# Optimization experiments

Measured on AMD Instinct MI355X. Metric: run time of the kernel, lower is better.

The kernel has to match this reference:

```python
import jax, jax.numpy as jnp
import numpy as np


def setup_inputs() -> dict:
    key = jax.random.key(0)
    k1, k2 = jax.random.split(key, 2)
    N, HrWr, HW = 16, 4096, 1024
    num_levels, max_k = 3, 5
    return {
        "R_combined": jax.random.normal(k1, (N, HrWr, HW), dtype=jnp.float32),
        "k_logits": jax.random.normal(k2, (num_levels, max_k), dtype=jnp.float32),
        "temperature": jnp.array(1.0, dtype=jnp.float32),
        "max_k": 5,
        "num_levels": 3,
    }


def reference(R_combined, k_logits, temperature, max_k, num_levels):
    # --- gumbel-softmax over k choices (soft samples, as in F.gumbel_softmax) ---
    gkey = jax.random.key(42)
    u = jax.random.uniform(gkey, k_logits.shape, k_logits.dtype,
                           minval=1e-6, maxval=1.0 - 1e-6)
    gumbels = -jnp.log(-jnp.log(u))
    k_probs = jax.nn.softmax((k_logits + gumbels) / temperature, axis=-1)  # [L, max_k]
    k_hard = jnp.argmax(k_probs, axis=-1) + 1                              # [L] ints in [1, max_k]
    k_soft = jnp.sum(k_probs * jnp.arange(1, max_k + 1, dtype=k_probs.dtype), axis=-1)
    # straight-through estimator
    k_selected = (jax.lax.stop_gradient(k_hard.astype(k_soft.dtype))
                  + k_soft - jax.lax.stop_gradient(k_soft))

    # --- top-k over HrWr axis (dim=1); take max_k once, then per-level mask.
    # topk(k) + pad to max_k with (-inf, 0)  ==  topk(max_k) masked at rank >= k,
    # since top_k returns sorted-descending values (matches torch.topk sorted=True).
    x = jnp.swapaxes(R_combined, 1, 2)           # [N, HW, HrWr]
    vals, idx = jax.lax.top_k(x, max_k)          # [N, HW, max_k]
    vals = jnp.swapaxes(vals, 1, 2)              # [N, max_k, HW]
    idx = jnp.swapaxes(idx, 1, 2)                # [N, max_k, HW]

    rank = jnp.arange(max_k)                     # [max_k]
    mask = (rank[None, :] < k_hard[:, None])[:, None, :, None]  # [L, 1, max_k, 1]
    R_star_levels = jnp.where(mask, vals[None], -jnp.inf)       # [L, N, max_k, HW]
    R_idx_levels = jnp.where(mask, idx[None], 0)                # [L, N, max_k, HW]

    return (k_selected, R_star_levels, R_idx_levels)
```

## Files before the change

kernel.cpp:

```cpp
#include <hip/hip_runtime.h>
#include <math.h>
#include <float.h>
#include <stdint.h>

#define N_N   16
#define HRWR  4096
#define HW_   1024
#define LVLS  3
#define MAXK  5
#define SEGS  8
#define SEGLEN (HRWR / SEGS)
#define COLS  32

#define NEG_SENTINEL (-1.0e30f)

__device__ __forceinline__ unsigned rotl32(unsigned x, unsigned r) {
  return (x << r) | (x >> (32u - r));
}

__device__ __forceinline__ bool beats(float v, int i, float V, int I) {
  return (v > V) || (v == V && i < I);
}

__global__ __launch_bounds__(256)
void dynk_kernel(const float* __restrict__ R,
                 const float* __restrict__ k_logits,
                 const float* __restrict__ temperature,
                 float* __restrict__ out)
{
  __shared__ float    s_vals[SEGS][COLS][MAXK];
  __shared__ int      s_idx [SEGS][COLS][MAXK];
  __shared__ unsigned s_bits[LVLS * MAXK];
  __shared__ int      s_khard[LVLS];

  const int tid = threadIdx.x;
  const int c   = tid & (COLS - 1);
  const int s   = tid >> 5;
  const int b   = blockIdx.x;
  const int n   = b >> 5;
  const int hw  = ((b & 31) << 5) | c;

  if (tid < LVLS * MAXK) {
    unsigned x0 = 0u, x1 = (unsigned)tid;
    const unsigned k0 = 0u, k1 = 42u;
    const unsigned k2 = k0 ^ k1 ^ 0x1BD11BDAu;
    x0 += k0; x1 += k1;
#define TF_RND(rot) { x0 += x1; x1 = rotl32(x1, rot); x1 ^= x0; }
    TF_RND(13) TF_RND(15) TF_RND(26) TF_RND(6)  x0 += k1; x1 += k2 + 1u;
    TF_RND(17) TF_RND(29) TF_RND(16) TF_RND(24) x0 += k2; x1 += k0 + 2u;
    TF_RND(13) TF_RND(15) TF_RND(26) TF_RND(6)  x0 += k0; x1 += k1 + 3u;
    TF_RND(17) TF_RND(29) TF_RND(16) TF_RND(24) x0 += k1; x1 += k2 + 4u;
    TF_RND(13) TF_RND(15) TF_RND(26) TF_RND(6)  x0 += k2; x1 += k0 + 5u;
#undef TF_RND
    s_bits[tid] = x0 ^ x1;
  }
  __syncthreads();

  if (tid == 0) {
    const float T = temperature[0];
    for (int l = 0; l < LVLS; ++l) {
      float z[MAXK], p[MAXK];
      float zmax = -INFINITY;
      for (int k = 0; k < MAXK; ++k) {
        unsigned bits = s_bits[l * MAXK + k];
        float f = __uint_as_float((bits >> 9) | 0x3f800000u) - 1.0f;
        const float mn = 1e-6f;
        const float mx = 1.0f - 1e-6f;
        float u = fmaxf(mn, f * (mx - mn) + mn);
        float g = -logf(-logf(u));
        z[k] = (k_logits[l * MAXK + k] + g) / T;
        zmax = fmaxf(zmax, z[k]);
      }
      float sum = 0.0f;
      for (int k = 0; k < MAXK; ++k) { p[k] = expf(z[k] - zmax); sum += p[k]; }
      float pmax = -INFINITY; int arg = 0; float ksoft = 0.0f;
      for (int k = 0; k < MAXK; ++k) {
        p[k] = p[k] / sum;
        if (p[k] > pmax) { pmax = p[k]; arg = k; }
        ksoft += p[k] * (float)(k + 1);
      }
      const int khard = arg + 1;
      s_khard[l] = khard;
      if (b == 0) out[l] = ((float)khard + ksoft) - ksoft;
    }
  }

  float tv[MAXK];
  int   ti[MAXK];
#pragma unroll
  for (int k = 0; k < MAXK; ++k) { tv[k] = -INFINITY; ti[k] = 0x7fffffff; }

  const float* __restrict__ base =
      R + ((size_t)n * HRWR + (size_t)s * SEGLEN) * HW_ + hw;
  const int r0 = s * SEGLEN;

  for (int r = 0; r < SEGLEN; r += 8) {
    float v[8];
#pragma unroll
    for (int j = 0; j < 8; ++j) v[j] = base[(size_t)(r + j) * HW_];
#pragma unroll
    for (int j = 0; j < 8; ++j) {
      const float val = v[j];
      if (val > tv[MAXK - 1]) {
        tv[MAXK - 1] = val;
        ti[MAXK - 1] = r0 + r + j;
#pragma unroll
        for (int k = MAXK - 1; k > 0; --k) {
          if (tv[k] > tv[k - 1]) {
            float tf = tv[k]; tv[k] = tv[k - 1]; tv[k - 1] = tf;
            int   tt = ti[k]; ti[k] = ti[k - 1]; ti[k - 1] = tt;
          }
        }
      }
    }
  }

#pragma unroll
  for (int k = 0; k < MAXK; ++k) { s_vals[s][c][k] = tv[k]; s_idx[s][c][k] = ti[k]; }
  __syncthreads();

  if (tid < COLS) {
    const int cc = tid;
    float fv[MAXK]; int fi[MAXK];
#pragma unroll
    for (int k = 0; k < MAXK; ++k) { fv[k] = s_vals[0][cc][k]; fi[k] = s_idx[0][cc][k]; }
    for (int ss = 1; ss < SEGS; ++ss) {
#pragma unroll
      for (int k = 0; k < MAXK; ++k) {
        const float v = s_vals[ss][cc][k];
        const int   i = s_idx [ss][cc][k];
        if (beats(v, i, fv[MAXK - 1], fi[MAXK - 1])) {
          fv[MAXK - 1] = v; fi[MAXK - 1] = i;
#pragma unroll
          for (int k2 = MAXK - 1; k2 > 0; --k2) {
            if (beats(fv[k2], fi[k2], fv[k2 - 1], fi[k2 - 1])) {
              float tf = fv[k2]; fv[k2] = fv[k2 - 1]; fv[k2 - 1] = tf;
              int   tt = fi[k2]; fi[k2] = fi[k2 - 1]; fi[k2 - 1] = tt;
            }
          }
        }
      }
    }

    const int hww = ((b & 31) << 5) | cc;
    float* __restrict__ star = out + LVLS;
    float* __restrict__ idxo = out + LVLS + (size_t)LVLS * N_N * MAXK * HW_;
#pragma unroll
    for (int l = 0; l < LVLS; ++l) {
      const int kh = s_khard[l];
#pragma unroll
      for (int k = 0; k < MAXK; ++k) {
        const bool on = (k < kh);
        const size_t off = (((size_t)l * N_N + n) * MAXK + k) * HW_ + hww;
        star[off] = on ? fv[k] : NEG_SENTINEL;
        idxo[off] = on ? (float)fi[k] : 0.0f;
      }
    }
  }
}

extern "C" void kernel_launch(void* const* d_in, const int* in_sizes, int n_in,
                              void* d_out, int out_size, void* d_ws, size_t ws_size,
                              hipStream_t stream) {
  const float* R    = (const float*)d_in[0];
  const float* kl   = (const float*)d_in[1];
  const float* temp = (const float*)d_in[2];
  float* out = (float*)d_out;

  dynk_kernel<<<dim3(512), dim3(256), 0, stream>>>(R, kl, temp, out);
}
```

Measured before the change: 410.3 us.

## Split top-k into partial and final kernels for more parallelism

The single 512-block kernel becomes a two-stage split-K reduction. The first kernel launches 2048 blocks, each scanning 512 rows for 64 columns, and writes per-split top-5 candidates to workspace. A second kernel merges the 8 splits per column, computes the gumbel k_hard values and writes the masked outputs. This fills the GPU far better for a memory-bound 256MB read, at the cost of an extra launch and some workspace traffic. Each wavefront now reads 64 contiguous floats (256B) per row.

After: 410.6 us. About the same (+0.1%).

```diff
diff --git a/kernel.cpp b/kernel.cpp
--- a/kernel.cpp
+++ b/kernel.cpp
@@ -8,9 +8,11 @@
 #define HW_   1024
 #define LVLS  3
 #define MAXK  5
-#define SEGS  8
-#define SEGLEN (HRWR / SEGS)
-#define COLS  32
+
+#define SLICES   16
+#define RSPLIT   8
+#define K1_SEGS  4
+#define K1_SEGLEN 128
 
 #define NEG_SENTINEL (-1.0e30f)
 
@@ -22,23 +24,92 @@
   return (v > V) || (v == V && i < I);
 }
 
+__global__ __launch_bounds__(256, 6)
+void dynk_partial(const float* __restrict__ R, float2* __restrict__ ws)
+{
+  __shared__ float s_vals[K1_SEGS][64][MAXK];
+  __shared__ int   s_idx [K1_SEGS][64][MAXK];
+
+  const int tid   = threadIdx.x;
+  const int c     = tid & 63;
+  const int s     = tid >> 6;
+  const int b     = blockIdx.x;
+  const int rs    = b & (RSPLIT - 1);
+  const int slice = (b >> 3) & (SLICES - 1);
+  const int n     = b >> 7;
+
+  const int r0 = rs * 512 + s * K1_SEGLEN;
+  const float* __restrict__ base =
+      R + ((size_t)n * HRWR + r0) * HW_ + slice * 64 + c;
+
+  float tv[MAXK]; int ti[MAXK];
+#pragma unroll
+  for (int k = 0; k < MAXK; ++k) { tv[k] = -INFINITY; ti[k] = 0x7fffffff; }
+
+  for (int r = 0; r < K1_SEGLEN; r += 8) {
+    float v[8];
+#pragma unroll
+    for (int j = 0; j < 8; ++j) v[j] = base[(size_t)(r + j) * HW_];
+#pragma unroll
+    for (int j = 0; j < 8; ++j) {
+      const float val = v[j];
+      if (val > tv[MAXK - 1]) {
+        tv[MAXK - 1] = val;
+        ti[MAXK - 1] = r0 + r + j;
+#pragma unroll
+        for (int k = MAXK - 1; k > 0; --k) {
+          if (tv[k] > tv[k - 1]) {
+            float tf = tv[k]; tv[k] = tv[k - 1]; tv[k - 1] = tf;
+            int   tt = ti[k]; ti[k] = ti[k - 1]; ti[k - 1] = tt;
+          }
+        }
+      }
+    }
+  }
+
+#pragma unroll
+  for (int k = 0; k < MAXK; ++k) { s_vals[s][c][k] = tv[k]; s_idx[s][c][k] = ti[k]; }
+  __syncthreads();
+
+  if (tid < 64) {
+    const int cc = tid;
+    float fv[MAXK]; int fi[MAXK];
+#pragma unroll
+    for (int k = 0; k < MAXK; ++k) { fv[k] = s_vals[0][cc][k]; fi[k] = s_idx[0][cc][k]; }
+    for (int ss = 1; ss < K1_SEGS; ++ss) {
+#pragma unroll
+      for (int k = 0; k < MAXK; ++k) {
+        const float v = s_vals[ss][cc][k];
+        const int   i = s_idx [ss][cc][k];
+        if (beats(v, i, fv[MAXK - 1], fi[MAXK - 1])) {
+          fv[MAXK - 1] = v; fi[MAXK - 1] = i;
+#pragma unroll
+          for (int k2 = MAXK - 1; k2 > 0; --k2) {
+            if (beats(fv[k2], fi[k2], fv[k2 - 1], fi[k2 - 1])) {
+              float tf = fv[k2]; fv[k2] = fv[k2 - 1]; fv[k2 - 1] = tf;
+              int   tt = fi[k2]; fi[k2] = fi[k2 - 1]; fi[k2 - 1] = tt;
+            }
+          }
+        }
+      }
+    }
+    float2* __restrict__ dst = ws + ((size_t)b * 64 + cc) * MAXK;
+#pragma unroll
+    for (int k = 0; k < MAXK; ++k)
+      dst[k] = make_float2(fv[k], __int_as_float(fi[k]));
+  }
+}
+
 __global__ __launch_bounds__(256)
-void dynk_kernel(const float* __restrict__ R,
-                 const float* __restrict__ k_logits,
-                 const float* __restrict__ temperature,
-                 float* __restrict__ out)
+void dynk_final(const float2* __restrict__ ws,
+                const float* __restrict__ k_logits,
+                const float* __restrict__ temperature,
+                float* __restrict__ out)
 {
-  __shared__ float    s_vals[SEGS][COLS][MAXK];
-  __shared__ int      s_idx [SEGS][COLS][MAXK];
   __shared__ unsigned s_bits[LVLS * MAXK];
   __shared__ int      s_khard[LVLS];
 
   const int tid = threadIdx.x;
-  const int c   = tid & (COLS - 1);
-  const int s   = tid >> 5;
-  const int b   = blockIdx.x;
-  const int n   = b >> 5;
-  const int hw  = ((b & 31) << 5) | c;
 
   if (tid < LVLS * MAXK) {
     unsigned x0 = 0u, x1 = (unsigned)tid;
@@ -81,80 +152,57 @@
       }
       const int khard = arg + 1;
       s_khard[l] = khard;
-      if (b == 0) out[l] = ((float)khard + ksoft) - ksoft;
-    }
-  }
-
-  float tv[MAXK];
-  int   ti[MAXK];
-#pragma unroll
-  for (int k = 0; k < MAXK; ++k) { tv[k] = -INFINITY; ti[k] = 0x7fffffff; }
-
-  const float* __restrict__ base =
-      R + ((size_t)n * HRWR + (size_t)s * SEGLEN) * HW_ + hw;
-  const int r0 = s * SEGLEN;
-
-  for (int r = 0; r < SEGLEN; r += 8) {
-    float v[8];
-#pragma unroll
-    for (int j = 0; j < 8; ++j) v[j] = base[(size_t)(r + j) * HW_];
-#pragma unroll
-    for (int j = 0; j < 8; ++j) {
-      const float val = v[j];
-      if (val > tv[MAXK - 1]) {
-        tv[MAXK - 1] = val;
-        ti[MAXK - 1] = r0 + r + j;
-#pragma unroll
-        for (int k = MAXK - 1; k > 0; --k) {
-          if (tv[k] > tv[k - 1]) {
-            float tf = tv[k]; tv[k] = tv[k - 1]; tv[k - 1] = tf;
-            int   tt = ti[k]; ti[k] = ti[k - 1]; ti[k - 1] = tt;
+      if (blockIdx.x == 0) out[l] = ((float)khard + ksoft) - ksoft;
+    }
+  }
+  __syncthreads();
+
+  const int g  = blockIdx.x * 256 + tid;
+  const int n  = g >> 10;
+  const int hw = g & (HW_ - 1);
+  const int slice = hw >> 6;
+  const int cc    = hw & 63;
+
+  const size_t lbase = (((size_t)n * SLICES + slice) * RSPLIT);
+
+  float fv[MAXK]; int fi[MAXK];
+  {
+    const float2* __restrict__ src = ws + (lbase * 64 + cc) * MAXK;
+#pragma unroll
+    for (int k = 0; k < MAXK; ++k) {
+      float2 e = src[k]; fv[k] = e.x; fi[k] = __float_as_int(e.y);
+    }
+  }
+  for (int rs = 1; rs < RSPLIT; ++rs) {
+    const float2* __restrict__ src = ws + (((lbase + rs) * 64) + cc) * MAXK;
+#pragma unroll
+    for (int k = 0; k < MAXK; ++k) {
+      float2 e = src[k];
+      const float v = e.x; const int i = __float_as_int(e.y);
+      if (beats(v, i, fv[MAXK - 1], fi[MAXK - 1])) {
+        fv[MAXK - 1] = v; fi[MAXK - 1] = i;
+#pragma unroll
+        for (int k2 = MAXK - 1; k2 > 0; --k2) {
+          if (beats(fv[k2], fi[k2], fv[k2 - 1], fi[k2 - 1])) {
+            float tf = fv[k2]; fv[k2] = fv[k2 - 1]; fv[k2 - 1] = tf;
+            int   tt = fi[k2]; fi[k2] = fi[k2 - 1]; fi[k2 - 1] = tt;
           }
         }
       }
     }
   }
 
-#pragma unroll
-  for (int k = 0; k < MAXK; ++k) { s_vals[s][c][k] = tv[k]; s_idx[s][c][k] = ti[k]; }
-  __syncthreads();
-
-  if (tid < COLS) {
-    const int cc = tid;
-    float fv[MAXK]; int fi[MAXK];
-#pragma unroll
-    for (int k = 0; k < MAXK; ++k) { fv[k] = s_vals[0][cc][k]; fi[k] = s_idx[0][cc][k]; }
-    for (int ss = 1; ss < SEGS; ++ss) {
-#pragma unroll
-      for (int k = 0; k < MAXK; ++k) {
-        const float v = s_vals[ss][cc][k];
-        const int   i = s_idx [ss][cc][k];
-        if (beats(v, i, fv[MAXK - 1], fi[MAXK - 1])) {
-          fv[MAXK - 1] = v; fi[MAXK - 1] = i;
-#pragma unroll
-          for (int k2 = MAXK - 1; k2 > 0; --k2) {
-            if (beats(fv[k2], fi[k2], fv[k2 - 1], fi[k2 - 1])) {
-              float tf = fv[k2]; fv[k2] = fv[k2 - 1]; fv[k2 - 1] = tf;
-              int   tt = fi[k2]; fi[k2] = fi[k2 - 1]; fi[k2 - 1] = tt;
-            }
-          }
-        }
-      }
-    }
-
-    const int hww = ((b & 31) << 5) | cc;
-    float* __restrict__ star = out + LVLS;
-    float* __restrict__ idxo = out + LVLS + (size_t)LVLS * N_N * MAXK * HW_;
-#pragma unroll
-    for (int l = 0; l < LVLS; ++l) {
-      const int kh = s_khard[l];
-#pragma unroll
-      for (int k = 0; k < MAXK; ++k) {
-        const bool on = (k < kh);
-        const size_t off = (((size_t)l * N_N + n) * MAXK + k) * HW_ + hww;
-        star[off] = on ? fv[k] : NEG_SENTINEL;
-        idxo[off] = on ? (float)fi[k] : 0.0f;
-      }
+  float* __restrict__ star = out + LVLS;
+  float* __restrict__ idxo = out + LVLS + (size_t)LVLS * N_N * MAXK * HW_;
+#pragma unroll
+  for (int l = 0; l < LVLS; ++l) {
+    const int kh = s_khard[l];
+#pragma unroll
+    for (int k = 0; k < MAXK; ++k) {
+      const bool on = (k < kh);
+      const size_t off = (((size_t)l * N_N + n) * MAXK + k) * HW_ + hw;
+      star[off] = on ? fv[k] : NEG_SENTINEL;
+      idxo[off] = on ? (float)fi[k] : 0.0f;
     }
   }
 }
@@ -165,7 +213,9 @@
   const float* R    = (const float*)d_in[0];
   const float* kl   = (const float*)d_in[1];
   const float* temp = (const float*)d_in[2];
-  float* out = (float*)d_out;
-
-  dynk_kernel<<<dim3(512), dim3(256), 0, stream>>>(R, kl, temp, out);
-}
+  float* out  = (float*)d_out;
+  float2* ws  = (float2*)d_ws;
+
+  dynk_partial<<<dim3(N_N * SLICES * RSPLIT), dim3(256), 0, stream>>>(R, ws);
+  dynk_final  <<<dim3((N_N * HW_) / 256), dim3(256), 0, stream>>>(ws, kl, temp, out);
+}
```
